# Kernel optimization log

Measured on AMD Instinct MI355X. Metric: run time of the kernel, lower is better.

## Reference

```python
import jax
import jax.numpy as jnp
from jax import lax
import numpy as np

HEADS = 12
GROUPS = 3
KSIZE = 5  # depthwise kernel for offset prediction


def bilinear_sample(img, grid):
    """img: (G,C,H,W); grid: (G,Hk,Wk,2) with (x,y) coords in [-1,1], align_corners=True.
    Returns (G,C,Hk*Wk). Coords are pre-clipped to [-1,1], so clamped indexing is exact."""
    G, C, H, W = img.shape
    gx = (grid[..., 0] + 1.0) * 0.5 * (W - 1)
    gy = (grid[..., 1] + 1.0) * 0.5 * (H - 1)
    x0 = jnp.floor(gx); y0 = jnp.floor(gy)
    wx1 = gx - x0; wx0 = 1.0 - wx1
    wy1 = gy - y0; wy0 = 1.0 - wy1
    x0i = jnp.clip(x0, 0, W - 1).astype(jnp.int32)
    x1i = jnp.clip(x0 + 1, 0, W - 1).astype(jnp.int32)
    y0i = jnp.clip(y0, 0, H - 1).astype(jnp.int32)
    y1i = jnp.clip(y0 + 1, 0, H - 1).astype(jnp.int32)
    flat = img.reshape(G, C, H * W)
    def gather(yi, xi):
        idx = (yi * W + xi).reshape(G, 1, -1)  # (G,1,Hk*Wk)
        return jnp.take_along_axis(flat, jnp.broadcast_to(idx, (G, C, idx.shape[-1])), axis=2)
    n = gx.shape[1] * gx.shape[2]
    w00 = (wy0 * wx0).reshape(G, 1, n); w01 = (wy0 * wx1).reshape(G, 1, n)
    w10 = (wy1 * wx0).reshape(G, 1, n); w11 = (wy1 * wx1).reshape(G, 1, n)
    return (gather(y0i, x0i) * w00 + gather(y0i, x1i) * w01 +
            gather(y1i, x0i) * w10 + gather(y1i, x1i) * w11)


def setup_inputs() -> dict:
    key = jax.random.key(0)
    ks = jax.random.split(key, 16)
    B, C, H, W = 8, 384, 32, 32
    Cg = C // GROUPS
    s = 0.02
    inp = {
        "x1": jax.random.normal(ks[0], (B, C, H, W), jnp.float32),
        "x2": jax.random.normal(ks[1], (B, C, H, W), jnp.float32),
        "wq": jax.random.normal(ks[2], (C, C), jnp.float32) * s,
        "bq": jnp.zeros((C,), jnp.float32),
        "w_off_dw": jax.random.normal(ks[3], (Cg, 1, KSIZE, KSIZE), jnp.float32) * s,
        "b_off_dw": jnp.zeros((Cg,), jnp.float32),
        "w_off_pw": jax.random.normal(ks[4], (2, Cg), jnp.float32) * s,
        "b_off_pw": jnp.zeros((2,), jnp.float32),
        "wk": jax.random.normal(ks[5], (C, C), jnp.float32) * s,
        "bk": jnp.zeros((C,), jnp.float32),
        "wv": jax.random.normal(ks[6], (C, C), jnp.float32) * s,
        "bv": jnp.zeros((C,), jnp.float32),
        "wo": jax.random.normal(ks[7], (C, C), jnp.float32) * s,
        "bo": jnp.zeros((C,), jnp.float32),
    }
    return inp


def deformable_cross_attn(x1, x2, wq, bq, w_off_dw, b_off_dw, w_off_pw, b_off_pw,
                          wk, bk, wv, bv, wo, bo):
    B, C, H, W = x1.shape
    Cg = C // GROUPS
    hc = C // HEADS
    scale = hc ** -0.5
    N = H * W
    # query projection (1x1 conv)
    q = jnp.einsum('oc,bchw->bohw', wq, x1) + bq[None, :, None, None]
    # grouped offset prediction: depthwise conv -> GELU -> 1x1 conv to 2 channels
    qg = q.reshape(B * GROUPS, Cg, H, W)
    off = lax.conv_general_dilated(qg, w_off_dw, (1, 1), 'SAME',
                                   feature_group_count=Cg,
                                   dimension_numbers=('NCHW', 'OIHW', 'NCHW'))
    off = jax.nn.gelu(off + b_off_dw[None, :, None, None])
    off = jnp.einsum('oc,bchw->bohw', w_off_pw, off) + b_off_pw[None, :, None, None]  # (B*G,2,H,W)
    dx = jnp.tanh(off[:, 0]) * (2.0 / W)
    dy = jnp.tanh(off[:, 1]) * (2.0 / H)
    ref_x = (jnp.arange(W, dtype=jnp.float32) + 0.5) / W * 2.0 - 1.0
    ref_y = (jnp.arange(H, dtype=jnp.float32) + 0.5) / H * 2.0 - 1.0
    px = jnp.clip(ref_x[None, None, :] + dx, -1.0, 1.0)
    py = jnp.clip(ref_y[None, :, None] + dy, -1.0, 1.0)
    grid = jnp.stack([px, py], axis=-1)  # (B*G,H,W,2)
    # sample key/value source at deformed positions
    x2g = x2.reshape(B * GROUPS, Cg, H, W)
    sampled = bilinear_sample(x2g, grid).reshape(B, C, N)
    k = jnp.einsum('oc,bcn->bon', wk, sampled) + bk[None, :, None]
    v = jnp.einsum('oc,bcn->bon', wv, sampled) + bv[None, :, None]
    qf = q.reshape(B, HEADS, hc, N)
    kf = k.reshape(B, HEADS, hc, N)
    vf = v.reshape(B, HEADS, hc, N)
    attn = jax.nn.softmax(jnp.einsum('bhcn,bhcm->bhnm', qf, kf) * scale, axis=-1)
    out = jnp.einsum('bhnm,bhcm->bhcn', attn, vf).reshape(B, C, H, W)
    y = jnp.einsum('oc,bchw->bohw', wo, out) + bo[None, :, None, None]
    return x1 + y, attn


def reference(x1, x2, wq, bq, w_off_dw, b_off_dw, w_off_pw, b_off_pw,
              wk, bk, wv, bv, wo, bo):
    return deformable_cross_attn(x1, x2, wq, bq, w_off_dw, b_off_dw,
                                 w_off_pw, b_off_pw, wk, bk, wv, bv, wo, bo)
```

## Files before the change

kernel.cpp:

```cpp
#include <hip/hip_runtime.h>
#include <hip/hip_bf16.h>

static constexpr int B = 8;
static constexpr int C = 384;
static constexpr int H = 32;
static constexpr int W = 32;
static constexpr int N = 1024;
static constexpr int Cg = 128;
static constexpr int HEADS = 12;
static constexpr int BG = 24;
static constexpr float SCALE = 0.17677669529663687f;

typedef short bf16x8 __attribute__((ext_vector_type(8)));
typedef float f32x4 __attribute__((ext_vector_type(4)));

__device__ __forceinline__ unsigned short bf16_bits(float x) {
    __hip_bfloat16 h = __float2bfloat16(x);
    return __builtin_bit_cast(unsigned short, h);
}
__device__ __forceinline__ float bf2f(unsigned short u) {
    return __builtin_bit_cast(float, ((unsigned)u) << 16);
}
__device__ __forceinline__ float fast_tanh(float x) {
    float e = __expf(2.0f * x);
    return 1.0f - 2.0f / (e + 1.0f);
}
__device__ __forceinline__ bf16x8 cvt8(const float* p) {
    float4 f0 = *(const float4*)p;
    float4 f1 = *(const float4*)(p + 4);
    bf16x8 v;
    v[0] = (short)bf16_bits(f0.x); v[1] = (short)bf16_bits(f0.y);
    v[2] = (short)bf16_bits(f0.z); v[3] = (short)bf16_bits(f0.w);
    v[4] = (short)bf16_bits(f1.x); v[5] = (short)bf16_bits(f1.y);
    v[6] = (short)bf16_bits(f1.z); v[7] = (short)bf16_bits(f1.w);
    return v;
}

__global__ __launch_bounds__(256) void prep_x1(const float* __restrict__ x1,
                                               unsigned short* __restrict__ x1T)
{
    __shared__ float tile[32][132];
    const int xi = blockIdx.x;
    const int tid = threadIdx.x;
    const int n0 = (xi & 7) * 128;
    const int t = xi >> 3;
    const int c0 = (t % 12) * 32;
    const int b = t / 12;
    {
        int c = tid >> 3, nq = (tid & 7) * 16;
        const float* sp = x1 + ((size_t)b*C + c0 + c)*N + n0 + nq;
        #pragma unroll
        for (int i = 0; i < 4; ++i)
            *(float4*)&tile[c][nq + 4*i] = *(const float4*)(sp + 4*i);
    }
    __syncthreads();
    {
        int n = tid >> 1, cb = (tid & 1) * 16;
        unsigned short* dp = x1T + ((size_t)b*N + n0 + n)*C + c0 + cb;
        #pragma unroll
        for (int half = 0; half < 2; ++half) {
            bf16x8 v;
            #pragma unroll
            for (int j = 0; j < 8; ++j)
                v[j] = (short)bf16_bits(tile[cb + half*8 + j][n]);
            *(bf16x8*)(dp + half*8) = v;
        }
    }
}

template<int MODE>
__global__ __launch_bounds__(256) void proj_mfma(const unsigned short* __restrict__ XT,
                                                 const float* __restrict__ Wb,
                                                 const float* __restrict__ bias,
                                                 const float* __restrict__ res,
                                                 void* __restrict__ out,
                                                 void* __restrict__ out2)
{
    __shared__ __align__(16) char smem[64*72*2*2];
    unsigned short* sA = (unsigned short*)smem;
    unsigned short* sB = sA + 64*72;
    float* ep = (float*)smem;

    const int tid = threadIdx.x;
    const int lane = tid & 63, w = tid >> 6;
    const int l15 = lane & 15, lq = lane >> 4;
    const int n0 = blockIdx.x * 64, o0 = blockIdx.y * 64, b = blockIdx.z;
    const int qn = (w & 1) * 32, qo = (w >> 1) * 32;

    const unsigned short* xg = XT + ((size_t)b*N + n0)*C;
    const float* wg = Wb + (size_t)o0*C;

    const f32x4 zero = {0.f, 0.f, 0.f, 0.f};
    f32x4 a00 = zero, a01 = zero, a10 = zero, a11 = zero;

    const int r = tid >> 2, c8 = (tid & 3) * 8;
    for (int c0 = 0; c0 < C; c0 += 64) {
        __syncthreads();
        *(bf16x8*)(sA + r*72 + c8)      = *(const bf16x8*)(xg + (size_t)r*C + c0 + c8);
        *(bf16x8*)(sA + r*72 + c8 + 32) = *(const bf16x8*)(xg + (size_t)r*C + c0 + c8 + 32);
        *(bf16x8*)(sB + r*72 + c8)      = cvt8(wg + (size_t)r*C + c0 + c8);
        *(bf16x8*)(sB + r*72 + c8 + 32) = cvt8(wg + (size_t)r*C + c0 + c8 + 32);
        __syncthreads();
        #pragma unroll
        for (int ks = 0; ks < 2; ++ks) {
            bf16x8 fa0 = *(const bf16x8*)(sA + (qn + l15)*72      + ks*32 + lq*8);
            bf16x8 fa1 = *(const bf16x8*)(sA + (qn + 16 + l15)*72 + ks*32 + lq*8);
            bf16x8 fb0 = *(const bf16x8*)(sB + (qo + l15)*72      + ks*32 + lq*8);
            bf16x8 fb1 = *(const bf16x8*)(sB + (qo + 16 + l15)*72 + ks*32 + lq*8);
            a00 = __builtin_amdgcn_mfma_f32_16x16x32_bf16(fa0, fb0, a00, 0, 0, 0);
            a01 = __builtin_amdgcn_mfma_f32_16x16x32_bf16(fa0, fb1, a01, 0, 0, 0);
            a10 = __builtin_amdgcn_mfma_f32_16x16x32_bf16(fa1, fb0, a10, 0, 0, 0);
            a11 = __builtin_amdgcn_mfma_f32_16x16x32_bf16(fa1, fb1, a11, 0, 0, 0);
        }
    }
    __syncthreads();
    #pragma unroll
    for (int rr = 0; rr < 4; ++rr) {
        int nr0 = qn + 4*lq + rr, nr1 = qn + 16 + 4*lq + rr;
        ep[nr0*65 + qo + l15]      = a00[rr];
        ep[nr0*65 + qo + 16 + l15] = a01[rr];
        ep[nr1*65 + qo + l15]      = a10[rr];
        ep[nr1*65 + qo + 16 + l15] = a11[rr];
    }
    __syncthreads();

    if constexpr (MODE == 3) {
        {
            int n = tid >> 2, ch = tid & 3;
            unsigned short* op = (unsigned short*)out + ((size_t)b*N + n0 + n)*C + o0;
            #pragma unroll
            for (int half = 0; half < 2; ++half) {
                int ob = ch*8 + half*32;
                bf16x8 v;
                #pragma unroll
                for (int j = 0; j < 8; ++j)
                    v[j] = (short)bf16_bits(ep[n*65 + ob + j] + bias[o0 + ob + j]);
                *(bf16x8*)(op + ob) = v;
            }
        }
        {
            int o = tid >> 2, nc = (tid & 3) * 16;
            float bz = bias[o0 + o];
            unsigned short* dp = (unsigned short*)out2 + ((size_t)b*C + o0 + o)*N + n0 + nc;
            #pragma unroll
            for (int half = 0; half < 2; ++half) {
                bf16x8 v;
                #pragma unroll
                for (int j = 0; j < 8; ++j)
                    v[j] = (short)bf16_bits(ep[(nc + half*8 + j)*65 + o] + bz);
                *(bf16x8*)(dp + half*8) = v;
            }
        }
    } else {
        int o = tid >> 2, nc = (tid & 3) * 16;
        float bz = bias[o0 + o];
        size_t base = ((size_t)b*C + o0 + o)*N + n0 + nc;
        #pragma unroll
        for (int i = 0; i < 4; ++i) {
            float4 rv = *(const float4*)(res + base + 4*i);
            f32x4 v;
            v[0] = ep[(nc + 4*i + 0)*65 + o] + bz + rv.x;
            v[1] = ep[(nc + 4*i + 1)*65 + o] + bz + rv.y;
            v[2] = ep[(nc + 4*i + 2)*65 + o] + bz + rv.z;
            v[3] = ep[(nc + 4*i + 3)*65 + o] + bz + rv.w;
            __builtin_nontemporal_store(v, (f32x4*)((float*)out + base + 4*i));
        }
    }
}

__global__ __launch_bounds__(256) void proj_kv(const unsigned short* __restrict__ XT,
                                               const float* __restrict__ Wk,
                                               const float* __restrict__ bk,
                                               const float* __restrict__ Wv,
                                               const float* __restrict__ bv,
                                               unsigned short* __restrict__ K16,
                                               unsigned short* __restrict__ V16)
{
    __shared__ __align__(16) char smem[64*72*2*3];
    unsigned short* sA  = (unsigned short*)smem;
    unsigned short* sBk = sA + 64*72;
    unsigned short* sBv = sA + 2*64*72;
    float* ep = (float*)smem;

    const int tid = threadIdx.x;
    const int lane = tid & 63, w = tid >> 6;
    const int l15 = lane & 15, lq = lane >> 4;
    const int n0 = blockIdx.x * 64, o0 = blockIdx.y * 64, b = blockIdx.z;
    const int qn = (w & 1) * 32, qo = (w >> 1) * 32;

    const unsigned short* xg = XT + ((size_t)b*N + n0)*C;
    const float* wkg = Wk + (size_t)o0*C;
    const float* wvg = Wv + (size_t)o0*C;

    const f32x4 zero = {0.f, 0.f, 0.f, 0.f};
    f32x4 k00 = zero, k01 = zero, k10 = zero, k11 = zero;
    f32x4 v00 = zero, v01 = zero, v10 = zero, v11 = zero;

    const int r = tid >> 2, c8 = (tid & 3) * 8;
    for (int c0 = 0; c0 < C; c0 += 64) {
        __syncthreads();
        *(bf16x8*)(sA  + r*72 + c8)      = *(const bf16x8*)(xg  + (size_t)r*C + c0 + c8);
        *(bf16x8*)(sA  + r*72 + c8 + 32) = *(const bf16x8*)(xg  + (size_t)r*C + c0 + c8 + 32);
        *(bf16x8*)(sBk + r*72 + c8)      = cvt8(wkg + (size_t)r*C + c0 + c8);
        *(bf16x8*)(sBk + r*72 + c8 + 32) = cvt8(wkg + (size_t)r*C + c0 + c8 + 32);
        *(bf16x8*)(sBv + r*72 + c8)      = cvt8(wvg + (size_t)r*C + c0 + c8);
        *(bf16x8*)(sBv + r*72 + c8 + 32) = cvt8(wvg + (size_t)r*C + c0 + c8 + 32);
        __syncthreads();
        #pragma unroll
        for (int ks = 0; ks < 2; ++ks) {
            bf16x8 fa0 = *(const bf16x8*)(sA + (qn + l15)*72      + ks*32 + lq*8);
            bf16x8 fa1 = *(const bf16x8*)(sA + (qn + 16 + l15)*72 + ks*32 + lq*8);
            bf16x8 fk0 = *(const bf16x8*)(sBk + (qo + l15)*72      + ks*32 + lq*8);
            bf16x8 fk1 = *(const bf16x8*)(sBk + (qo + 16 + l15)*72 + ks*32 + lq*8);
            bf16x8 fv0 = *(const bf16x8*)(sBv + (qo + l15)*72      + ks*32 + lq*8);
            bf16x8 fv1 = *(const bf16x8*)(sBv + (qo + 16 + l15)*72 + ks*32 + lq*8);
            k00 = __builtin_amdgcn_mfma_f32_16x16x32_bf16(fa0, fk0, k00, 0, 0, 0);
            k01 = __builtin_amdgcn_mfma_f32_16x16x32_bf16(fa0, fk1, k01, 0, 0, 0);
            k10 = __builtin_amdgcn_mfma_f32_16x16x32_bf16(fa1, fk0, k10, 0, 0, 0);
            k11 = __builtin_amdgcn_mfma_f32_16x16x32_bf16(fa1, fk1, k11, 0, 0, 0);
            v00 = __builtin_amdgcn_mfma_f32_16x16x32_bf16(fa0, fv0, v00, 0, 0, 0);
            v01 = __builtin_amdgcn_mfma_f32_16x16x32_bf16(fa0, fv1, v01, 0, 0, 0);
            v10 = __builtin_amdgcn_mfma_f32_16x16x32_bf16(fa1, fv0, v10, 0, 0, 0);
            v11 = __builtin_amdgcn_mfma_f32_16x16x32_bf16(fa1, fv1, v11, 0, 0, 0);
        }
    }
    __syncthreads();
    #pragma unroll
    for (int rr = 0; rr < 4; ++rr) {
        int nr0 = qn + 4*lq + rr, nr1 = qn + 16 + 4*lq + rr;
        ep[nr0*65 + qo + l15]      = k00[rr];
        ep[nr0*65 + qo + 16 + l15] = k01[rr];
        ep[nr1*65 + qo + l15]      = k10[rr];
        ep[nr1*65 + qo + 16 + l15] = k11[rr];
    }
    __syncthreads();
    {
        int n = tid >> 2, ch = tid & 3;
        unsigned short* op = K16 + ((size_t)b*N + n0 + n)*C + o0;
        #pragma unroll
        for (int half = 0; half < 2; ++half) {
            int ob = ch*8 + half*32;
            bf16x8 v;
            #pragma unroll
            for (int j = 0; j < 8; ++j)
                v[j] = (short)bf16_bits((ep[n*65 + ob + j] + bk[o0 + ob + j]) * SCALE);
            *(bf16x8*)(op + ob) = v;
        }
    }
    __syncthreads();
    #pragma unroll
    for (int rr = 0; rr < 4; ++rr) {
        int nr0 = qn + 4*lq + rr, nr1 = qn + 16 + 4*lq + rr;
        ep[nr0*65 + qo + l15]      = v00[rr];
        ep[nr0*65 + qo + 16 + l15] = v01[rr];
        ep[nr1*65 + qo + l15]      = v10[rr];
        ep[nr1*65 + qo + 16 + l15] = v11[rr];
    }
    __syncthreads();
    {
        int o = tid >> 2, nc = (tid & 3) * 16;
        float bz = bv[o0 + o];
        unsigned short* op = V16 + ((size_t)b*C + o0 + o)*N + n0 + nc;
        #pragma unroll
        for (int half = 0; half < 2; ++half) {
            bf16x8 v;
            #pragma unroll
            for (int j = 0; j < 8; ++j)
                v[j] = (short)bf16_bits(ep[(nc + half*8 + j)*65 + o] + bz);
            *(bf16x8*)(op + half*8) = v;
        }
    }
}

__global__ __launch_bounds__(256) void dwconv_gelu(const unsigned short* __restrict__ q,
                                                   const float* __restrict__ wdw,
                                                   const float* __restrict__ bdw,
                                                   unsigned short* __restrict__ t)
{
    __shared__ float tile[12][32];
    __shared__ float wsm[25];
    const int bx = blockIdx.x;
    const int c = blockIdx.y, bg = blockIdx.z;
    const int tid = threadIdx.x;
    const unsigned short* qc = q + ((size_t)bg*Cg + c)*N;
    if (tid < 384) {
        int row = tid >> 5, col = tid & 31;
        int gy = bx*8 - 2 + row;
        tile[row][col] = (gy >= 0 && gy < H) ? bf2f(qc[gy*W + col]) : 0.0f;
    }
    if (tid < 25) wsm[tid] = wdw[c*25 + tid];
    __syncthreads();
    const int yl = tid >> 5, x = tid & 31;
    float acc = bdw[c];
    #pragma unroll
    for (int ky = 0; ky < 5; ++ky) {
        #pragma unroll
        for (int kx = 0; kx < 5; ++kx) {
            int xx = x + kx - 2;
            if (xx < 0 || xx >= W) continue;
            acc += wsm[ky*5 + kx] * tile[yl + ky][xx];
        }
    }
    float u = acc;
    float g = 0.5f*u*(1.0f + fast_tanh(0.7978845608028654f*(u + 0.044715f*u*u*u)));
    t[((size_t)bg*Cg + c)*N + bx*256 + tid] = bf16_bits(g);
}

__global__ __launch_bounds__(256) void offbilin(const unsigned short* __restrict__ t,
                                                const float* __restrict__ wpw,
                                                const float* __restrict__ bpw,
                                                const float* __restrict__ x2,
                                                unsigned short* __restrict__ sampT)
{
    __shared__ float r0[4][64], r1[4][64];
    __shared__ float4 cbuf[64];
    __shared__ unsigned short st[64][130];
    const int tid = threadIdx.x;
    const int n0 = blockIdx.x * 64, bg = blockIdx.y;
    const int nl = tid & 63, cq = tid >> 6;
    {
        const unsigned short* tb = t + ((size_t)bg*Cg + cq*32)*N + n0 + nl;
        float a0 = 0.f, a1 = 0.f;
        #pragma unroll 8
        for (int i = 0; i < 32; ++i) {
            float tv = bf2f(tb[(size_t)i*N]);
            a0 += wpw[cq*32 + i] * tv;
            a1 += wpw[Cg + cq*32 + i] * tv;
        }
        r0[cq][nl] = a0; r1[cq][nl] = a1;
    }
    __syncthreads();
    if (tid < 64) {
        int n = n0 + nl;
        const int x = n & 31, y = n >> 5;
        float a0 = bpw[0] + r0[0][nl] + r0[1][nl] + r0[2][nl] + r0[3][nl];
        float a1 = bpw[1] + r1[0][nl] + r1[1][nl] + r1[2][nl] + r1[3][nl];
        float dx = fast_tanh(a0) * (2.0f / W);
        float dy = fast_tanh(a1) * (2.0f / H);
        float rx = (x + 0.5f) / W * 2.0f - 1.0f;
        float ry = (y + 0.5f) / H * 2.0f - 1.0f;
        float px = fminf(fmaxf(rx + dx, -1.0f), 1.0f);
        float py = fminf(fmaxf(ry + dy, -1.0f), 1.0f);
        float gx = (px + 1.0f) * 0.5f * (W - 1);
        float gy = (py + 1.0f) * 0.5f * (H - 1);
        float x0 = floorf(gx), y0 = floorf(gy);
        float wx1 = gx - x0, wy1 = gy - y0;
        x0 = fminf(fmaxf(x0, 0.0f), (float)(W - 1));
        y0 = fminf(fmaxf(y0, 0.0f), (float)(H - 1));
        cbuf[nl] = make_float4(x0, y0, wx1, wy1);
    }
    __syncthreads();
    {
        float4 c4 = cbuf[nl];
        int x0 = (int)c4.x, y0 = (int)c4.y;
        float wx1 = c4.z, wy1 = c4.w;
        int x1 = min(x0 + 1, W - 1), y1 = min(y0 + 1, H - 1);
        float wx0 = 1.0f - wx1, wy0 = 1.0f - wy1;
        const float* base = x2 + (size_t)bg*Cg*N;
        #pragma unroll 4
        for (int i = 0; i < 32; ++i) {
            int c = cq*32 + i;
            const float* img = base + (size_t)c*N;
            float v00 = img[y0*W + x0], v01 = img[y0*W + x1];
            float v10 = img[y1*W + x0], v11 = img[y1*W + x1];
            float v = wy0*(wx0*v00 + wx1*v01) + wy1*(wx0*v10 + wx1*v11);
            st[nl][c] = bf16_bits(v);
        }
    }
    __syncthreads();
    {
        int b = bg / 3, g = bg % 3;
        int nn = tid >> 2;
        unsigned short* dp = sampT + ((size_t)b*N + n0 + nn)*C + g*Cg;
        #pragma unroll
        for (int i = 0; i < 4; ++i) {
            int c8 = ((tid & 3) + 4*i) * 8;
            *(bf16x8*)(dp + c8) = *(const bf16x8*)&st[nn][c8];
        }
    }
}

__global__ __launch_bounds__(256) void attn_fused(const unsigned short* __restrict__ Q16,
                                                  const unsigned short* __restrict__ K16,
                                                  const unsigned short* __restrict__ V16,
                                                  float* __restrict__ attn,
                                                  unsigned short* __restrict__ OT)
{
    __shared__ __align__(16) unsigned short smem[33024 + 4608];
    unsigned short* ks = smem;
    unsigned short* vs = smem;
    unsigned short* ps = smem + 33024;

    const int tid = threadIdx.x;
    const int lane = tid & 63, w = tid >> 6;
    const int l15 = lane & 15, lq = lane >> 4;
    const int id = blockIdx.x;
    const int xcd = id & 7, j = id >> 3;
    const int bh = xcd*12 + (j >> 4);
    const int nb = j & 15;
    const int b = bh / HEADS, h = bh - b*HEADS;

    const unsigned short* qg = Q16 + ((size_t)b*N + nb*64)*C + h*32;
    const unsigned short* kg = K16 + (size_t)b*N*C + h*32;
    const unsigned short* vg = V16 + ((size_t)b*C + h*32)*N;

    const bf16x8 qfrag = *(const bf16x8*)(qg + (size_t)(w*16 + l15)*C + lq*8);

    const f32x4 zero = {0.f, 0.f, 0.f, 0.f};
    unsigned int pp[128];
    float sm = 0.f;

    #pragma unroll
    for (int ch = 0; ch < 4; ++ch) {
        __syncthreads();
        #pragma unroll
        for (int i = 0; i < 4; ++i) {
            int m = i*64 + (tid >> 2), c8 = (tid & 3) * 8;
            *(bf16x8*)(ks + m*40 + c8) = *(const bf16x8*)(kg + ((size_t)ch*256 + m)*C + c8);
        }
        __syncthreads();
        #pragma unroll
        for (int tg = 0; tg < 4; ++tg) {
            f32x4 s[4];
            #pragma unroll
            for (int i = 0; i < 4; ++i) {
                bf16x8 kfrag = *(const bf16x8*)(ks + (16*(tg*4+i) + l15)*40 + lq*8);
                s[i] = __builtin_amdgcn_mfma_f32_16x16x32_bf16(kfrag, qfrag, zero, 0, 0, 0);
            }
            #pragma unroll
            for (int i = 0; i < 4; ++i) {
                float e0 = __expf(s[i][0]), e1 = __expf(s[i][1]);
                float e2 = __expf(s[i][2]), e3 = __expf(s[i][3]);
                sm += (e0 + e1) + (e2 + e3);
                pp[ch*32 + (tg*4+i)*2 + 0] = (unsigned)bf16_bits(e0) | ((unsigned)bf16_bits(e1) << 16);
                pp[ch*32 + (tg*4+i)*2 + 1] = (unsigned)bf16_bits(e2) | ((unsigned)bf16_bits(e3) << 16);
            }
        }
    }
    sm += __shfl_xor(sm, 16);
    sm += __shfl_xor(sm, 32);
    const float inv = 1.0f / sm;

    __syncthreads();
    #pragma unroll
    for (int i = 0; i < 16; ++i) {
        int u = tid + i*256;
        int cl = u >> 7, gg = u & 127;
        *(bf16x8*)(vs + cl*1032 + gg*8) = *(const bf16x8*)(vg + (size_t)cl*N + gg*8);
    }
    __syncthreads();

    f32x4 outf[2] = {zero, zero};
    unsigned short* pw = ps + w*16*72;
    float* abase = attn + ((size_t)bh*N + (size_t)nb*64 + w*16)*N;
    const int trow = lane >> 4;
    const int tcol = (lane & 15) * 4;

    #pragma unroll
    for (int ch = 0; ch < 4; ++ch) {
        #pragma unroll
        for (int qr = 0; qr < 4; ++qr) {
            #pragma unroll
            for (int tt = 0; tt < 4; ++tt) {
                int t = qr*4 + tt;
                uint2 pb;
                pb.x = pp[ch*32 + t*2];
                pb.y = pp[ch*32 + t*2 + 1];
                *(uint2*)(pw + l15*72 + 16*tt + 4*lq) = pb;
            }
            __asm volatile("" ::: "memory");
            #pragma unroll
            for (int kk = 0; kk < 2; ++kk) {
                bf16x8 pa = *(const bf16x8*)(pw + l15*72 + kk*32 + lq*8);
                #pragma unroll
                for (int ct = 0; ct < 2; ++ct) {
                    bf16x8 vb = *(const bf16x8*)(vs + (16*ct + l15)*1032 + ch*256 + qr*64 + kk*32 + lq*8);
                    outf[ct] = __builtin_amdgcn_mfma_f32_16x16x32_bf16(pa, vb, outf[ct], 0, 0, 0);
                }
            }
            #pragma unroll
            for (int it = 0; it < 4; ++it) {
                int row = it*4 + trow;
                uint2 u = *(const uint2*)(pw + row*72 + tcol);
                float invr = __shfl(inv, row);
                f32x4 p;
                p[0] = __builtin_bit_cast(float, u.x << 16) * invr;
                p[1] = __builtin_bit_cast(float, u.x & 0xffff0000u) * invr;
                p[2] = __builtin_bit_cast(float, u.y << 16) * invr;
                p[3] = __builtin_bit_cast(float, u.y & 0xffff0000u) * invr;
                __builtin_nontemporal_store(p,
                    (f32x4*)(abase + (size_t)row*N + ch*256 + qr*64 + tcol));
            }
            __asm volatile("" ::: "memory");
        }
    }

    float* sc = (float*)pw;
    #pragma unroll
    for (int r = 0; r < 4; ++r) {
        float invr = __shfl(inv, 4*lq + r);
        sc[(4*lq + r)*33 + l15]      = outf[0][r] * invr;
        sc[(4*lq + r)*33 + 16 + l15] = outf[1][r] * invr;
    }
    __asm volatile("" ::: "memory");
    {
        int n = lane >> 2, c8 = (lane & 3) * 8;
        bf16x8 v;
        #pragma unroll
        for (int j2 = 0; j2 < 8; ++j2)
            v[j2] = (short)bf16_bits(sc[n*33 + c8 + j2]);
        *(bf16x8*)(OT + ((size_t)b*N + nb*64 + w*16 + n)*C + h*32 + c8) = v;
    }
}

extern "C" void kernel_launch(void* const* d_in, const int* in_sizes, int n_in,
                              void* d_out, int out_size, void* d_ws, size_t ws_size,
                              hipStream_t stream)
{
    const float* x1  = (const float*)d_in[0];
    const float* x2  = (const float*)d_in[1];
    const float* wq  = (const float*)d_in[2];
    const float* bq  = (const float*)d_in[3];
    const float* wdw = (const float*)d_in[4];
    const float* bdw = (const float*)d_in[5];
    const float* wpw = (const float*)d_in[6];
    const float* bpw = (const float*)d_in[7];
    const float* wk  = (const float*)d_in[8];
    const float* bk  = (const float*)d_in[9];
    const float* wv  = (const float*)d_in[10];
    const float* bv  = (const float*)d_in[11];
    const float* wo  = (const float*)d_in[12];
    const float* bo  = (const float*)d_in[13];

    const size_t P = (size_t)B * C * N;
    float* ws = (float*)d_ws;
    unsigned short* Q16   = (unsigned short*)ws;
    unsigned short* qspat = (unsigned short*)(ws + P/2);
    unsigned short* sampT = (unsigned short*)(ws + P);
    unsigned short* K16   = (unsigned short*)(ws + 3*P/2);
    unsigned short* V16   = (unsigned short*)(ws + 2*P);
    unsigned short* x1T   = (unsigned short*)(ws + 5*P/2);
    unsigned short* OT    = x1T;
    unsigned short* tbuf  = (unsigned short*)(ws + 3*P);

    float* ybuf = (float*)d_out;
    float* attn = (float*)d_out + P;

    prep_x1<<<dim3(768), 256, 0, stream>>>(x1, x1T);
    proj_mfma<3><<<dim3(16, 6, 8), 256, 0, stream>>>(x1T, wq, bq, nullptr, Q16, qspat);
    dwconv_gelu<<<dim3(4, Cg, BG), 256, 0, stream>>>(qspat, wdw, bdw, tbuf);
    offbilin<<<dim3(16, BG), 256, 0, stream>>>(tbuf, wpw, bpw, x2, sampT);
    proj_kv<<<dim3(16, 6, 8), 256, 0, stream>>>(sampT, wk, bk, wv, bv, K16, V16);
    attn_fused<<<dim3(1536), 256, 0, stream>>>(Q16, K16, V16, attn, OT);
    proj_mfma<2><<<dim3(16, 6, 8), 256, 0, stream>>>(OT, wo, bo, x1, ybuf, nullptr);
}
```

Measured before the change: 179.5 us.

## Recompute QK scores in second pass instead of holding probabilities in registers

The attention kernel no longer keeps all 128 packed bf16 probabilities per thread in registers between the sum pass and the output pass. It now recomputes the QK^T MFMA and exp in the second pass, reloading K chunks alongside chunked V tiles. LDS shrinks from a full 32x1024 V staging buffer to a per-chunk 32x256 tile. This cuts register and LDS pressure to raise occupancy, but it doubles the QK MFMA and exp work and the K loads.

```diff
diff --git a/kernel.cpp b/kernel.cpp
--- a/kernel.cpp
+++ b/kernel.cpp
@@ -386,10 +386,9 @@
                                                   float* __restrict__ attn,
                                                   unsigned short* __restrict__ OT)
 {
-    __shared__ __align__(16) unsigned short smem[33024 + 4608];
-    unsigned short* ks = smem;
-    unsigned short* vs = smem;
-    unsigned short* ps = smem + 33024;
+    __shared__ __align__(16) unsigned short ks[256*40];
+    __shared__ __align__(16) unsigned short vs[32*264];
+    __shared__ __align__(16) unsigned short ps[4][16*72];
 
     const int tid = threadIdx.x;
     const int lane = tid & 63, w = tid >> 6;
@@ -407,10 +406,9 @@
     const bf16x8 qfrag = *(const bf16x8*)(qg + (size_t)(w*16 + l15)*C + lq*8);
 
     const f32x4 zero = {0.f, 0.f, 0.f, 0.f};
-    unsigned int pp[128];
     float sm = 0.f;
-
-    #pragma unroll
+    f32x4 s[16];
+
     for (int ch = 0; ch < 4; ++ch) {
         __syncthreads();
         #pragma unroll
@@ -420,52 +418,57 @@
         }
         __syncthreads();
         #pragma unroll
-        for (int tg = 0; tg < 4; ++tg) {
-            f32x4 s[4];
-            #pragma unroll
-            for (int i = 0; i < 4; ++i) {
-                bf16x8 kfrag = *(const bf16x8*)(ks + (16*(tg*4+i) + l15)*40 + lq*8);
-                s[i] = __builtin_amdgcn_mfma_f32_16x16x32_bf16(kfrag, qfrag, zero, 0, 0, 0);
-            }
-            #pragma unroll
-            for (int i = 0; i < 4; ++i) {
-                float e0 = __expf(s[i][0]), e1 = __expf(s[i][1]);
-                float e2 = __expf(s[i][2]), e3 = __expf(s[i][3]);
-                sm += (e0 + e1) + (e2 + e3);
-                pp[ch*32 + (tg*4+i)*2 + 0] = (unsigned)bf16_bits(e0) | ((unsigned)bf16_bits(e1) << 16);
-                pp[ch*32 + (tg*4+i)*2 + 1] = (unsigned)bf16_bits(e2) | ((unsigned)bf16_bits(e3) << 16);
-            }
-        }
+        for (int t = 0; t < 16; ++t) {
+            bf16x8 kfrag = *(const bf16x8*)(ks + (16*t + l15)*40 + lq*8);
+            s[t] = __builtin_amdgcn_mfma_f32_16x16x32_bf16(kfrag, qfrag, zero, 0, 0, 0);
+        }
+        float es = 0.f;
+        #pragma unroll
+        for (int t = 0; t < 16; ++t) {
+            es += __expf(s[t][0]); es += __expf(s[t][1]);
+            es += __expf(s[t][2]); es += __expf(s[t][3]);
+        }
+        sm += es;
     }
     sm += __shfl_xor(sm, 16);
     sm += __shfl_xor(sm, 32);
     const float inv = 1.0f / sm;
 
-    __syncthreads();
-    #pragma unroll
-    for (int i = 0; i < 16; ++i) {
-        int u = tid + i*256;
-        int cl = u >> 7, gg = u & 127;
-        *(bf16x8*)(vs + cl*1032 + gg*8) = *(const bf16x8*)(vg + (size_t)cl*N + gg*8);
-    }
-    __syncthreads();
-
     f32x4 outf[2] = {zero, zero};
-    unsigned short* pw = ps + w*16*72;
+    unsigned short* pw = ps[w];
     float* abase = attn + ((size_t)bh*N + (size_t)nb*64 + w*16)*N;
     const int trow = lane >> 4;
     const int tcol = (lane & 15) * 4;
 
-    #pragma unroll
     for (int ch = 0; ch < 4; ++ch) {
+        __syncthreads();
+        #pragma unroll
+        for (int i = 0; i < 4; ++i) {
+            int m = i*64 + (tid >> 2), c8 = (tid & 3) * 8;
+            *(bf16x8*)(ks + m*40 + c8) = *(const bf16x8*)(kg + ((size_t)ch*256 + m)*C + c8);
+        }
+        #pragma unroll
+        for (int i = 0; i < 4; ++i) {
+            int u = tid + i*256;
+            int cl = u >> 5, gg = u & 31;
+            *(bf16x8*)(vs + cl*264 + gg*8) = *(const bf16x8*)(vg + (size_t)cl*N + ch*256 + gg*8);
+        }
+        __syncthreads();
+        #pragma unroll
+        for (int t = 0; t < 16; ++t) {
+            bf16x8 kfrag = *(const bf16x8*)(ks + (16*t + l15)*40 + lq*8);
+            s[t] = __builtin_amdgcn_mfma_f32_16x16x32_bf16(kfrag, qfrag, zero, 0, 0, 0);
+        }
         #pragma unroll
         for (int qr = 0; qr < 4; ++qr) {
             #pragma unroll
             for (int tt = 0; tt < 4; ++tt) {
                 int t = qr*4 + tt;
+                float e0 = __expf(s[t][0]), e1 = __expf(s[t][1]);
+                float e2 = __expf(s[t][2]), e3 = __expf(s[t][3]);
                 uint2 pb;
-                pb.x = pp[ch*32 + t*2];
-                pb.y = pp[ch*32 + t*2 + 1];
+                pb.x = (unsigned)bf16_bits(e0) | ((unsigned)bf16_bits(e1) << 16);
+                pb.y = (unsigned)bf16_bits(e2) | ((unsigned)bf16_bits(e3) << 16);
                 *(uint2*)(pw + l15*72 + 16*tt + 4*lq) = pb;
             }
             __asm volatile("" ::: "memory");
@@ -474,7 +477,7 @@
                 bf16x8 pa = *(const bf16x8*)(pw + l15*72 + kk*32 + lq*8);
                 #pragma unroll
                 for (int ct = 0; ct < 2; ++ct) {
-                    bf16x8 vb = *(const bf16x8*)(vs + (16*ct + l15)*1032 + ch*256 + qr*64 + kk*32 + lq*8);
+                    bf16x8 vb = *(const bf16x8*)(vs + (16*ct + l15)*264 + qr*64 + kk*32 + lq*8);
                     outf[ct] = __builtin_amdgcn_mfma_f32_16x16x32_bf16(pa, vb, outf[ct], 0, 0, 0);
                 }
             }
```

After: 174.4 us. -2.9%, faster.
